# Kernel optimization log

Measured on AMD Instinct MI355X. Metric: run time of the kernel, lower is better.

Reference implementation:

```python
import jax, jax.numpy as jnp
import numpy as np

B, P, H = 256, 100, 512
NH, HD = 16, 32          # n_head, head_dim
V, N = 20, 200
VN = 1 + V + N           # 221
CSD = 16                 # cur_status_dim
SCALE = HD ** (-0.5)


def setup_inputs() -> dict:
    key = jax.random.key(0)
    ks = jax.random.split(key, 16)
    inp = {
        "q_global": jax.random.normal(ks[0], (B, P, H), jnp.float32),
        "k_global": jax.random.normal(ks[1], (B, NH, VN, HD), jnp.float32),
        "v_global": jax.random.normal(ks[2], (B, NH, VN, HD), jnp.float32),
        "k_node": jax.random.normal(ks[3], (B, NH, 1 + N, HD), jnp.float32),
        "v_node": jax.random.normal(ks[4], (B, NH, 1 + N, HD), jnp.float32),
        "k_vehicle": jax.random.normal(ks[5], (B, NH, 1 + V, HD), jnp.float32),
        "v_vehicle": jax.random.normal(ks[6], (B, NH, 1 + V, HD), jnp.float32),
        "k_vehicle_node": jax.random.normal(ks[7], (B, NH, V, HD), jnp.float32),
        "v_vehicle_node": jax.random.normal(ks[8], (B, NH, V, HD), jnp.float32),
        "context_feature": jax.random.normal(ks[9], (B, P, CSD), jnp.float32),
        "cache_pointer": jax.random.normal(ks[10], (B, H, VN), jnp.float32),
    }
    # random illegal mask; keep the depot column (0) always legal so no row is fully masked
    mask = jax.random.bernoulli(ks[11], 0.3, (B * P, VN))
    inp["illegal_mask"] = mask.at[:, 0].set(False)
    # learned params (torch Linear stores [out, in])
    inp["Wq_w"] = jax.random.normal(ks[12], (H, H + CSD), jnp.float32) * 0.02
    inp["combine_w"] = jax.random.normal(ks[13], (H, H), jnp.float32) * 0.02
    inp["combine_b"] = jax.random.normal(ks[14], (H,), jnp.float32) * 0.02
    return inp


def _attend(q, k, v, mask=None):
    # q: [B,NH,P,HD], k/v: [B,NH,K,HD], mask: [B,P,K] bool (True = illegal)
    scores = jnp.einsum("bhpd,bhkd->bhpk", q, k) * SCALE
    if mask is not None:
        scores = jnp.where(mask[:, None, :, :], -jnp.inf, scores)
    w = jax.nn.softmax(scores, axis=-1)
    ctx = jnp.einsum("bhpk,bhkd->bhpd", w, v)
    return ctx.transpose(0, 2, 1, 3).reshape(q.shape[0], q.shape[2], NH * HD)  # [B,P,H]


def reference(q_global, k_global, v_global, k_node, v_node, k_vehicle, v_vehicle,
              k_vehicle_node, v_vehicle_node, context_feature, cache_pointer,
              illegal_mask, Wq_w, combine_w, combine_b):
    mask = illegal_mask.reshape(B, P, VN)
    q = jnp.concatenate([q_global, context_feature], axis=-1) @ Wq_w.T  # [B,P,H]
    q = q.reshape(B, P, NH, HD).transpose(0, 2, 1, 3)                   # [B,NH,P,HD]
    context = (_attend(q, k_global, v_global, mask)
               + _attend(q, k_node, v_node)
               + _attend(q, k_vehicle, v_vehicle)
               + _attend(q, k_vehicle_node, v_vehicle_node))            # [B,P,H]
    mha_out = context @ combine_w.T + combine_b                          # [B,P,H]
    logits = jnp.einsum("bph,bhk->bpk", mha_out, cache_pointer)          # [B,P,VN]
    return logits.reshape(B * P, VN).astype(jnp.float32)
```

## Files before the change

kernel.cpp:

```cpp
#include <hip/hip_runtime.h>
#include <hip/hip_bf16.h>

#define B_   256
#define P_   100
#define H_   512
#define NH_  16
#define HD_  32
#define VN_  221
#define KNODE 201
#define KVEH  21
#define KVND  20
#define CSD_ 16
#define MASKP 224

typedef __attribute__((ext_vector_type(8))) short short8;
typedef __attribute__((ext_vector_type(4))) float f32x4;

#define K_OFF   0
#define V_OFF   38400
#define ATTN_LDS_B 69632

__device__ __forceinline__ unsigned cvtpk(float lo, float hi) {
    unsigned r;
    asm("v_cvt_pk_bf16_f32 %0, %1, %2" : "=v"(r) : "v"(lo), "v"(hi));
    return r;
}
__device__ __forceinline__ unsigned f2bf(float f) {
    union { float f; unsigned u; } x; x.f = f;
    return (x.u + 0x7FFFu + ((x.u >> 16) & 1u)) >> 16;
}

__global__ void mask_detect_kernel(const unsigned int* __restrict__ w,
                                   int nwords, int* __restrict__ flag) {
    int i = blockIdx.x * 256 + threadIdx.x;
    if (i < nwords && (w[i] & ~1u)) atomicOr(flag, 1);
}

__global__ void mask_repack_kernel(const unsigned char* __restrict__ mb,
                                   const int* __restrict__ mw,
                                   const int* __restrict__ flag,
                                   unsigned char* __restrict__ out) {
    int i = blockIdx.x * blockDim.x + threadIdx.x;
    if (i >= B_ * P_ * MASKP) return;
    int row = i / MASKP, k = i - row * MASKP;
    unsigned char v = 1;
    if (k < VN_) {
        int src = row * VN_ + k;
        v = (*flag) ? (unsigned char)(mb[src] != 0) : (unsigned char)(mw[src] != 0);
    }
    out[i] = v;
}

template<bool MASKED, int C0, int C1, int LO, int HI>
__device__ __forceinline__ void attend_v5(
    const char* __restrict__ ldsb,
    const unsigned* __restrict__ mpre,
    short8 qf, int g, int qr, int addrA, int addrB,
    f32x4& O0, f32x4& O1)
{
    f32x4 A0a = {0.f,0.f,0.f,0.f}, A1a = {0.f,0.f,0.f,0.f};
    f32x4 A0b = {0.f,0.f,0.f,0.f}, A1b = {0.f,0.f,0.f,0.f};
    float ssum = 0.f;
    const bool sel = g < 2;
    #pragma unroll
    for (int c = C0; c <= C1; ++c) {
        const int kb = c * 32;
        short8 kf0 = *(const short8*)(ldsb + K_OFF + (size_t)(kb + qr) * 80 + g * 16);
        short8 kf1 = *(const short8*)(ldsb + K_OFF + (size_t)(kb + 16 + qr) * 80 + g * 16);
        __builtin_amdgcn_s_setprio(1);
        f32x4 s0 = __builtin_amdgcn_mfma_f32_16x16x32_bf16(
                       kf0, qf, (f32x4){0.f,0.f,0.f,0.f}, 0, 0, 0);
        f32x4 s1 = __builtin_amdgcn_mfma_f32_16x16x32_bf16(
                       kf1, qf, (f32x4){0.f,0.f,0.f,0.f}, 0, 0, 0);
        __builtin_amdgcn_s_setprio(0);
        unsigned mdw0 = 0, mdw1 = 0;
        if (MASKED) {
            mdw0 = mpre[2 * (c - C0)];
            mdw1 = mpre[2 * (c - C0) + 1];
        }
        float e0[4], e1[4];
        #pragma unroll
        for (int r = 0; r < 4; ++r) {
            const int key0 = kb + 4 * g + r;
            const int key1 = key0 + 16;
            float x0 = exp2f(s0[r]);
            float x1 = exp2f(s1[r]);
            bool ok0, ok1;
            if (MASKED) {
                ok0 = ((mdw0 >> (8 * r)) & 255u) == 0u;
                ok1 = ((mdw1 >> (8 * r)) & 255u) == 0u;
            } else {
                ok0 = (key0 >= LO) & (key0 < HI);
                ok1 = (key1 >= LO) & (key1 < HI);
            }
            e0[r] = ok0 ? x0 : 0.f;
            e1[r] = ok1 ? x1 : 0.f;
            ssum += e0[r] + e1[r];
        }
        unsigned w0 = cvtpk(e0[0], e0[1]), w1 = cvtpk(e0[2], e0[3]);
        unsigned w2 = cvtpk(e1[0], e1[1]), w3 = cvtpk(e1[2], e1[3]);
        int pA0 = __builtin_amdgcn_ds_bpermute(addrA, (int)w0);
        int pA1 = __builtin_amdgcn_ds_bpermute(addrA, (int)w1);
        int pB0 = __builtin_amdgcn_ds_bpermute(addrB, (int)w0);
        int pB1 = __builtin_amdgcn_ds_bpermute(addrB, (int)w1);
        int qA0 = __builtin_amdgcn_ds_bpermute(addrA, (int)w2);
        int qA1 = __builtin_amdgcn_ds_bpermute(addrA, (int)w3);
        int qB0 = __builtin_amdgcn_ds_bpermute(addrB, (int)w2);
        int qB1 = __builtin_amdgcn_ds_bpermute(addrB, (int)w3);
        union { int u[4]; short8 s8; } pf;
        pf.u[0] = sel ? pA0 : qA0;
        pf.u[1] = sel ? pA1 : qA1;
        pf.u[2] = sel ? pB0 : qB0;
        pf.u[3] = sel ? pB1 : qB1;
        short8 v0 = *(const short8*)(ldsb + V_OFF + (size_t)qr * 976 + kb * 2 + g * 16);
        short8 v1 = *(const short8*)(ldsb + V_OFF + (size_t)(qr + 16) * 976 + kb * 2 + g * 16);
        __builtin_amdgcn_s_setprio(1);
        if (c & 1) {
            A0b = __builtin_amdgcn_mfma_f32_16x16x32_bf16(v0, pf.s8, A0b, 0, 0, 0);
            A1b = __builtin_amdgcn_mfma_f32_16x16x32_bf16(v1, pf.s8, A1b, 0, 0, 0);
        } else {
            A0a = __builtin_amdgcn_mfma_f32_16x16x32_bf16(v0, pf.s8, A0a, 0, 0, 0);
            A1a = __builtin_amdgcn_mfma_f32_16x16x32_bf16(v1, pf.s8, A1a, 0, 0, 0);
        }
        __builtin_amdgcn_s_setprio(0);
    }
    ssum += __shfl_xor(ssum, 16);
    ssum += __shfl_xor(ssum, 32);
    const float inv = 1.f / ssum;
    O0 += (A0a + A0b) * inv;
    O1 += (A1a + A1b) * inv;
}

__global__ __launch_bounds__(512, 4) void attn_mfma_kernel(
    const float* __restrict__ q4,
    const float* __restrict__ kg,  const float* __restrict__ vg,
    const float* __restrict__ kn,  const float* __restrict__ vn,
    const float* __restrict__ kv,  const float* __restrict__ vv,
    const float* __restrict__ kvn, const float* __restrict__ vvn,
    const unsigned char* __restrict__ maskp,
    float* __restrict__ ctx_out)
{
    extern __shared__ char ldsb[];
    const int tid = threadIdx.x;
    const int bh = blockIdx.x, b = bh >> 4, nh = bh & 15;

    const int wave = tid >> 6;
    const int g = (tid >> 4) & 3, qr = tid & 15;
    const int q0 = wave * 16;
    const int qe = (q0 + qr < 100) ? (q0 + qr) : 99;
    const float* qp = q4 + ((size_t)bh * 100 + qe) * 32 + g * 8;
    float4 qa = *(const float4*)qp;
    float4 qc = *(const float4*)(qp + 4);
    const unsigned char* mrow = maskp + ((size_t)b * 100 + qe) * MASKP;
    unsigned mpre[14];
    #pragma unroll
    for (int c = 0; c < 7; ++c) {
        mpre[2 * c]     = *(const unsigned*)(mrow + c * 32 + g * 4);
        mpre[2 * c + 1] = *(const unsigned*)(mrow + c * 32 + 16 + g * 4);
    }

    const float* kg_s  = kg  + (size_t)bh * VN_   * 32;
    const float* kn_s  = kn  + (size_t)bh * KNODE * 32;
    const float* kv_s  = kv  + (size_t)bh * KVEH  * 32;
    const float* kvn_s = kvn + (size_t)bh * KVND  * 32;
    const float* vg_s  = vg  + (size_t)bh * VN_   * 32;
    const float* vn_s  = vn  + (size_t)bh * KNODE * 32;
    const float* vv_s  = vv  + (size_t)bh * KVEH  * 32;
    const float* vvn_s = vvn + (size_t)bh * KVND  * 32;

    {
        float4 ka[4], kc[4];
        int koff[4]; bool kok[4];
        #pragma unroll
        for (int it = 0; it < 4; ++it) {
            int slot = tid + it * 512;
            kok[it] = slot < 1852;
            const float* sp; int li, r0;
            if (slot >= 1772)      { sp = kvn_s; li = slot - 1772; r0 = 456; }
            else if (slot >= 1688) { sp = kv_s;  li = slot - 1688; r0 = 432; }
            else if (slot >= 884)  { sp = kn_s;  li = slot - 884;  r0 = 224; }
            else                   { sp = kg_s;  li = slot;        r0 = 0;   }
            int r = li >> 2, s2 = li & 3;
            koff[it] = (r0 + r) * 80 + s2 * 16;
            if (kok[it]) {
                ka[it] = *(const float4*)(sp + r * 32 + s2 * 8);
                kc[it] = *(const float4*)(sp + r * 32 + s2 * 8 + 4);
            }
        }
        #pragma unroll
        for (int it = 0; it < 4; ++it) {
            if (kok[it]) {
                uint4 w;
                w.x = cvtpk(ka[it].x, ka[it].y); w.y = cvtpk(ka[it].z, ka[it].w);
                w.z = cvtpk(kc[it].x, kc[it].y); w.w = cvtpk(kc[it].z, kc[it].w);
                *(uint4*)(ldsb + K_OFF + koff[it]) = w;
            }
        }
    }
    for (int lin = tid; lin < 17 * 4; lin += 512) {
        int zi = lin >> 2, s = lin & 3;
        int zr = (zi < 3) ? 221 + zi : (zi < 10) ? 422 + zi
               : (zi < 13) ? 443 + zi : 463 + zi;
        *(uint4*)(ldsb + K_OFF + (size_t)zr * 80 + s * 16) = (uint4){0,0,0,0};
    }
    {
        char* vb = ldsb + V_OFF;
        float4 va[4], vb4[4];
        int vd0[4], vk2[4]; bool vok[4];
        #pragma unroll
        for (int it = 0; it < 4; ++it) {
            int slot = tid + it * 512;
            vok[it] = slot < 1840;
            const float* sp; int li, r0;
            if (slot >= 1760)      { sp = vvn_s; li = slot - 1760; r0 = 456; }
            else if (slot >= 1680) { sp = vv_s;  li = slot - 1680; r0 = 432; }
            else if (slot >= 880)  { sp = vn_s;  li = slot - 880;  r0 = 224; }
            else                   { sp = vg_s;  li = slot;        r0 = 0;   }
            int p = li >> 3, dq = li & 7;
            vd0[it] = dq * 4;
            vk2[it] = (r0 + 2 * p) * 2;
            if (vok[it]) {
                va[it]  = *(const float4*)(sp + (2 * p) * 32 + dq * 4);
                vb4[it] = *(const float4*)(sp + (2 * p + 1) * 32 + dq * 4);
            }
        }
        #pragma unroll
        for (int it = 0; it < 4; ++it) {
            if (vok[it]) {
                int d0 = vd0[it], k2 = vk2[it];
                *(unsigned*)(vb + (size_t)(d0 + 0) * 976 + k2) = cvtpk(va[it].x, vb4[it].x);
                *(unsigned*)(vb + (size_t)(d0 + 1) * 976 + k2) = cvtpk(va[it].y, vb4[it].y);
                *(unsigned*)(vb + (size_t)(d0 + 2) * 976 + k2) = cvtpk(va[it].z, vb4[it].z);
                *(unsigned*)(vb + (size_t)(d0 + 3) * 976 + k2) = cvtpk(va[it].w, vb4[it].w);
            }
        }
        if (tid < 32) {
            int d = tid;
            *(unsigned*)(vb + (size_t)d * 976 + 220 * 2) = cvtpk(vg_s[220 * 32 + d], 0.f);
            *(unsigned*)(vb + (size_t)d * 976 + 424 * 2) = cvtpk(vn_s[200 * 32 + d], 0.f);
            *(unsigned*)(vb + (size_t)d * 976 + 452 * 2) = cvtpk(vv_s[20 * 32 + d], 0.f);
        }
        for (int lin = tid; lin < 7 * 32; lin += 512) {
            int pi = lin >> 5, d = lin & 31;
            int pk = (pi == 0) ? 222 : (pi < 4) ? 424 + 2 * pi
                   : (pi == 4) ? 454 : 466 + 2 * pi;
            *(unsigned*)(vb + (size_t)d * 976 + (size_t)pk * 2) = 0;
        }
    }
    __syncthreads();

    if (wave >= 7) return;

    short8 qf;
    {
        const float SC = 0.2550524218f;
        union { unsigned u[4]; short8 s8; } q;
        q.u[0] = cvtpk(qa.x * SC, qa.y * SC);
        q.u[1] = cvtpk(qa.z * SC, qa.w * SC);
        q.u[2] = cvtpk(qc.x * SC, qc.y * SC);
        q.u[3] = cvtpk(qc.z * SC, qc.w * SC);
        qf = q.s8;
    }
    const int addrA = 4 * (qr + ((g & 1) << 5));
    const int addrB = addrA + 64;

    f32x4 O0 = {0.f,0.f,0.f,0.f}, O1 = {0.f,0.f,0.f,0.f};
    attend_v5<true,  0,  6,   0, 224>(ldsb, mpre, qf, g, qr, addrA, addrB, O0, O1);
    attend_v5<false, 7, 13, 224, 425>(ldsb, nullptr, qf, g, qr, addrA, addrB, O0, O1);
    attend_v5<false,13, 14, 432, 453>(ldsb, nullptr, qf, g, qr, addrA, addrB, O0, O1);
    attend_v5<false,14, 14, 456, 476>(ldsb, nullptr, qf, g, qr, addrA, addrB, O0, O1);

    if (q0 + qr < 100) {
        float* op = ctx_out + ((size_t)b * 100 + q0 + qr) * 512 + nh * 32 + 4 * g;
        *(f32x4*)op        = O0;
        *(f32x4*)(op + 16) = O1;
    }
}

template<bool QPROJ>
__global__ __launch_bounds__(512, 4) void gemm_nfused(
    const float* __restrict__ Aq, const float* __restrict__ cf,
    const float* __restrict__ W,  const float* __restrict__ bias,
    float* __restrict__ outp)
{
    __shared__ char As[64 * 80];
    __shared__ char Bs[256 * 80];
    const int tid = threadIdx.x;
    const int n0 = blockIdx.x * 256, m0 = blockIdx.y * 64;
    const int wave = tid >> 6, lane = tid & 63;
    const int wm = wave >> 2, wn = wave & 3;
    const int g = lane >> 4, qr = lane & 15;
    const int ar = tid >> 3, as = tid & 7;
    constexpr int KTOT_ = QPROJ ? 544 : 512;
    constexpr int WSTR  = QPROJ ? 528 : 512;

    f32x4 acc[2][4] = {};
    for (int k0 = 0; k0 < KTOT_; k0 += 32) {
        float4 a4 = {0,0,0,0};
        {
            const int k = k0 + as * 4;
            if (!QPROJ || k < 512) {
                a4 = *(const float4*)(Aq + (size_t)(m0 + ar) * 512 + k);
            } else if (k < 528) {
                a4 = *(const float4*)(cf + (size_t)(m0 + ar) * 16 + (k - 512));
            }
        }
        float4 b0[2], b1[2];
        #pragma unroll
        for (int it = 0; it < 2; ++it) {
            int slot = tid + it * 512;
            int row = slot >> 2, sq = slot & 3;
            int k = k0 + sq * 8;
            b0[it] = (float4){0,0,0,0}; b1[it] = (float4){0,0,0,0};
            if (!QPROJ || k < 528) {
                const float* wp = W + (size_t)(n0 + row) * WSTR + k;
                b0[it] = *(const float4*)wp;
                b1[it] = *(const float4*)(wp + 4);
            }
        }
        __syncthreads();
        {
            uint2 w;
            w.x = cvtpk(a4.x, a4.y); w.y = cvtpk(a4.z, a4.w);
            *(uint2*)(As + ar * 80 + as * 8) = w;
        }
        #pragma unroll
        for (int it = 0; it < 2; ++it) {
            int slot = tid + it * 512;
            int row = slot >> 2, sq = slot & 3;
            uint4 w;
            w.x = cvtpk(b0[it].x, b0[it].y); w.y = cvtpk(b0[it].z, b0[it].w);
            w.z = cvtpk(b1[it].x, b1[it].y); w.w = cvtpk(b1[it].z, b1[it].w);
            *(uint4*)(Bs + row * 80 + sq * 16) = w;
        }
        __syncthreads();
        short8 af0 = *(const short8*)(As + (wm * 32 + qr) * 80 + g * 16);
        short8 af1 = *(const short8*)(As + (wm * 32 + 16 + qr) * 80 + g * 16);
        #pragma unroll
        for (int nj = 0; nj < 4; ++nj) {
            short8 bf = *(const short8*)(Bs + (wn * 64 + nj * 16 + qr) * 80 + g * 16);
            acc[0][nj] = __builtin_amdgcn_mfma_f32_16x16x32_bf16(af0, bf, acc[0][nj], 0, 0, 0);
            acc[1][nj] = __builtin_amdgcn_mfma_f32_16x16x32_bf16(af1, bf, acc[1][nj], 0, 0, 0);
        }
    }
    #pragma unroll
    for (int mi = 0; mi < 2; ++mi)
        #pragma unroll
        for (int nj = 0; nj < 4; ++nj) {
            const int n = n0 + wn * 64 + nj * 16 + qr;
            const float bia = QPROJ ? 0.f : bias[n];
            #pragma unroll
            for (int reg = 0; reg < 4; ++reg) {
                int m = m0 + wm * 32 + 16 * mi + 4 * g + reg;
                if (QPROJ) {
                    int bb = m / 100, p = m - bb * 100;
                    int nh = n >> 5, d = n & 31;
                    outp[(((size_t)bb * NH_ + nh) * P_ + p) * HD_ + d] = acc[mi][nj][reg];
                } else {
                    outp[(size_t)m * 512 + n] = acc[mi][nj][reg] + bia;
                }
            }
        }
}

__global__ __launch_bounds__(512, 4) void logits_mfma(
    const float* __restrict__ mha,
    const float* __restrict__ cp,
    float* __restrict__ out)
{
    __shared__ char As[128 * 80];
    __shared__ char Bs[112 * 80];
    const int b   = blockIdx.x >> 1;
    const int nh0 = (blockIdx.x & 1) * 112;
    const int tid = threadIdx.x;
    const int wave = tid >> 6, lane = tid & 63;
    const int g = lane >> 4, qr = lane & 15;
    const int row = tid >> 2, s = tid & 3;

    f32x4 acc[7] = {};
    for (int h0 = 0; h0 < 512; h0 += 32) {
        float4 a4 = {0,0,0,0}, c4 = {0,0,0,0};
        if (row < 100) {
            const float* mp = mha + ((size_t)b * P_ + row) * 512 + h0 + 8 * s;
            a4 = *(const float4*)mp;
            c4 = *(const float4*)(mp + 4);
        }
        float cv[2][4];
        int ckk[2], chq[2]; bool cok[2];
        #pragma unroll
        for (int it = 0; it < 2; ++it) {
            int slot = tid + it * 512;
            bool in = slot < 896;
            int kkl = in ? (slot % 112) : 0;
            int hq  = in ? (slot / 112) : 0;
            int kk  = nh0 + kkl;
            ckk[it] = kkl; chq[it] = hq;
            cok[it] = in;
            cv[it][0] = cv[it][1] = cv[it][2] = cv[it][3] = 0.f;
            if (in && kk < VN_) {
                const float* cpp = cp + ((size_t)b * 512 + h0 + hq * 4) * VN_ + kk;
                cv[it][0] = cpp[0];
                cv[it][1] = cpp[VN_];
                cv[it][2] = cpp[2 * VN_];
                cv[it][3] = cpp[3 * VN_];
            }
        }
        __syncthreads();
        {
            uint4 w;
            w.x = cvtpk(a4.x, a4.y); w.y = cvtpk(a4.z, a4.w);
            w.z = cvtpk(c4.x, c4.y); w.w = cvtpk(c4.z, c4.w);
            *(uint4*)(As + row * 80 + s * 16) = w;
        }
        #pragma unroll
        for (int it = 0; it < 2; ++it) {
            if (cok[it]) {
                uint2 w;
                w.x = cvtpk(cv[it][0], cv[it][1]);
                w.y = cvtpk(cv[it][2], cv[it][3]);
                *(uint2*)(Bs + ckk[it] * 80 + chq[it] * 8) = w;
            }
        }
        __syncthreads();
        short8 af = *(const short8*)(As + (wave * 16 + qr) * 80 + g * 16);
        #pragma unroll
        for (int ni = 0; ni < 7; ++ni) {
            short8 bf = *(const short8*)(Bs + (ni * 16 + qr) * 80 + g * 16);
            acc[ni] = __builtin_amdgcn_mfma_f32_16x16x32_bf16(af, bf, acc[ni], 0, 0, 0);
        }
    }
    #pragma unroll
    for (int ni = 0; ni < 7; ++ni) {
        int key = nh0 + ni * 16 + qr;
        if (key >= VN_) continue;
        #pragma unroll
        for (int reg = 0; reg < 4; ++reg) {
            int p = wave * 16 + 4 * g + reg;
            if (p < P_)
                out[((size_t)b * P_ + p) * VN_ + key] = acc[ni][reg];
        }
    }
}

extern "C" void kernel_launch(void* const* d_in, const int* in_sizes, int n_in,
                              void* d_out, int out_size, void* d_ws, size_t ws_size,
                              hipStream_t stream) {
    const float* qg   = (const float*)d_in[0];
    const float* kgl  = (const float*)d_in[1];
    const float* vgl  = (const float*)d_in[2];
    const float* knd  = (const float*)d_in[3];
    const float* vnd  = (const float*)d_in[4];
    const float* kvh  = (const float*)d_in[5];
    const float* vvh  = (const float*)d_in[6];
    const float* kvnd = (const float*)d_in[7];
    const float* vvnd = (const float*)d_in[8];
    const float* cf   = (const float*)d_in[9];
    const float* cp   = (const float*)d_in[10];
    const void*  mask_raw = d_in[11];
    const float* Wq   = (const float*)d_in[12];
    const float* Wc   = (const float*)d_in[13];
    const float* bias = (const float*)d_in[14];
    float* out = (float*)d_out;

    const size_t NQ = (size_t)B_ * NH_ * P_ * HD_;
    float* q4buf  = (float*)d_ws;
    float* ctxbuf = q4buf + NQ;
    float* mhabuf = q4buf;
    unsigned char* mask8 = (unsigned char*)(ctxbuf + NQ);
    const int MASKN_P = B_ * P_ * MASKP;
    int* flag = (int*)(mask8 + ((MASKN_P + 15) & ~15));

    hipFuncSetAttribute(reinterpret_cast<const void*>(attn_mfma_kernel),
                        hipFuncAttributeMaxDynamicSharedMemorySize,
                        ATTN_LDS_B);

    hipMemsetAsync(flag, 0, sizeof(int), stream);
    mask_detect_kernel<<<16, 256, 0, stream>>>(
        (const unsigned int*)mask_raw, 4096, flag);
    mask_repack_kernel<<<(MASKN_P + 255) / 256, 256, 0, stream>>>(
        (const unsigned char*)mask_raw, (const int*)mask_raw, flag, mask8);

    gemm_nfused<true><<<dim3(2, 400), 512, 0, stream>>>(qg, cf, Wq, nullptr, q4buf);
    attn_mfma_kernel<<<B_ * NH_, 512, ATTN_LDS_B, stream>>>(
        q4buf, kgl, vgl, knd, vnd, kvh, vvh, kvnd, vvnd, mask8, ctxbuf);
    gemm_nfused<false><<<dim3(2, 400), 512, 0, stream>>>(ctxbuf, nullptr, Wc, bias, mhabuf);
    logits_mfma<<<B_ * 2, 512, 0, stream>>>(mhabuf, cp, out);
}
```

Measured before the change: 337.6 us.

## Make attention kernel persistent with warp-specialized double-buffered K/V prefetch

Replaces the one-block-per-(batch,head) attention launch with 256 persistent 1024-thread blocks that each loop over 16 (batch,head) tiles. Seven waves compute attention on the current LDS buffer while the other nine waves load and convert the next tile's K/V into a second LDS buffer, with one barrier per iteration. This aims to hide the global-load and bf16-conversion latency behind the MFMA work. The cost is double the LDS per block (about 136 KB), so only one block fits per CU. Only 256 blocks are launched, which may leave some CUs idle, and the loop adds a per-tile barrier.

```diff
diff --git a/kernel.cpp b/kernel.cpp
--- a/kernel.cpp
+++ b/kernel.cpp
@@ -19,6 +19,7 @@
 #define K_OFF   0
 #define V_OFF   38400
 #define ATTN_LDS_B 69632
+#define ATTN_LDS_2B (2 * ATTN_LDS_B)
 
 __device__ __forceinline__ unsigned cvtpk(float lo, float hi) {
     unsigned r;
@@ -131,7 +132,7 @@
     O1 += (A1a + A1b) * inv;
 }
 
-__global__ __launch_bounds__(512, 4) void attn_mfma_kernel(
+__global__ __launch_bounds__(1024, 4) void attn_ws(
     const float* __restrict__ q4,
     const float* __restrict__ kg,  const float* __restrict__ vg,
     const float* __restrict__ kn,  const float* __restrict__ vn,
@@ -140,40 +141,42 @@
     const unsigned char* __restrict__ maskp,
     float* __restrict__ ctx_out)
 {
-    extern __shared__ char ldsb[];
+    extern __shared__ char lds2[];
     const int tid = threadIdx.x;
-    const int bh = blockIdx.x, b = bh >> 4, nh = bh & 15;
-
-    const int wave = tid >> 6;
-    const int g = (tid >> 4) & 3, qr = tid & 15;
+    const int wave = tid >> 6, g = (tid >> 4) & 3, qr = tid & 15;
     const int q0 = wave * 16;
     const int qe = (q0 + qr < 100) ? (q0 + qr) : 99;
-    const float* qp = q4 + ((size_t)bh * 100 + qe) * 32 + g * 8;
-    float4 qa = *(const float4*)qp;
-    float4 qc = *(const float4*)(qp + 4);
-    const unsigned char* mrow = maskp + ((size_t)b * 100 + qe) * MASKP;
-    unsigned mpre[14];
+    const int addrA = 4 * (qr + ((g & 1) << 5));
+    const int addrB = addrA + 64;
+    const int t0i = blockIdx.x;
+
     #pragma unroll
-    for (int c = 0; c < 7; ++c) {
-        mpre[2 * c]     = *(const unsigned*)(mrow + c * 32 + g * 4);
-        mpre[2 * c + 1] = *(const unsigned*)(mrow + c * 32 + 16 + g * 4);
-    }
-
-    const float* kg_s  = kg  + (size_t)bh * VN_   * 32;
-    const float* kn_s  = kn  + (size_t)bh * KNODE * 32;
-    const float* kv_s  = kv  + (size_t)bh * KVEH  * 32;
-    const float* kvn_s = kvn + (size_t)bh * KVND  * 32;
-    const float* vg_s  = vg  + (size_t)bh * VN_   * 32;
-    const float* vn_s  = vn  + (size_t)bh * KNODE * 32;
-    const float* vv_s  = vv  + (size_t)bh * KVEH  * 32;
-    const float* vvn_s = vvn + (size_t)bh * KVND  * 32;
+    for (int bi = 0; bi < 2; ++bi) {
+        char* ldsb = lds2 + bi * ATTN_LDS_B;
+        if (tid < 68) {
+            int zi = tid >> 2, s = tid & 3;
+            int zr = (zi < 3) ? 221 + zi : (zi < 10) ? 422 + zi
+                   : (zi < 13) ? 443 + zi : 463 + zi;
+            *(uint4*)(ldsb + K_OFF + (size_t)zr * 80 + s * 16) = (uint4){0,0,0,0};
+        }
+        char* vb = ldsb + V_OFF;
+        if (tid < 224) {
+            int pi = tid >> 5, d = tid & 31;
+            int pk = (pi == 0) ? 222 : (pi < 4) ? 424 + 2 * pi
+                   : (pi == 4) ? 454 : 466 + 2 * pi;
+            *(unsigned*)(vb + (size_t)d * 976 + (size_t)pk * 2) = 0;
+        }
+    }
 
     {
-        float4 ka[4], kc[4];
-        int koff[4]; bool kok[4];
-        #pragma unroll
-        for (int it = 0; it < 4; ++it) {
-            int slot = tid + it * 512;
+        const float* kg_s  = kg  + (size_t)t0i * VN_   * 32;
+        const float* kn_s  = kn  + (size_t)t0i * KNODE * 32;
+        const float* kv_s  = kv  + (size_t)t0i * KVEH  * 32;
+        const float* kvn_s = kvn + (size_t)t0i * KVND  * 32;
+        float4 ka[2], kc[2]; int koff[2]; bool kok[2];
+        #pragma unroll
+        for (int it = 0; it < 2; ++it) {
+            int slot = tid + it * 1024;
             kok[it] = slot < 1852;
             const float* sp; int li, r0;
             if (slot >= 1772)      { sp = kvn_s; li = slot - 1772; r0 = 456; }
@@ -188,28 +191,23 @@
             }
         }
         #pragma unroll
-        for (int it = 0; it < 4; ++it) {
+        for (int it = 0; it < 2; ++it) {
             if (kok[it]) {
                 uint4 w;
                 w.x = cvtpk(ka[it].x, ka[it].y); w.y = cvtpk(ka[it].z, ka[it].w);
                 w.z = cvtpk(kc[it].x, kc[it].y); w.w = cvtpk(kc[it].z, kc[it].w);
-                *(uint4*)(ldsb + K_OFF + koff[it]) = w;
-            }
-        }
-    }
-    for (int lin = tid; lin < 17 * 4; lin += 512) {
-        int zi = lin >> 2, s = lin & 3;
-        int zr = (zi < 3) ? 221 + zi : (zi < 10) ? 422 + zi
-               : (zi < 13) ? 443 + zi : 463 + zi;
-        *(uint4*)(ldsb + K_OFF + (size_t)zr * 80 + s * 16) = (uint4){0,0,0,0};
-    }
-    {
-        char* vb = ldsb + V_OFF;
-        float4 va[4], vb4[4];
-        int vd0[4], vk2[4]; bool vok[4];
-        #pragma unroll
-        for (int it = 0; it < 4; ++it) {
-            int slot = tid + it * 512;
+                *(uint4*)(lds2 + K_OFF + koff[it]) = w;
+            }
+        }
+        const float* vg_s  = vg  + (size_t)t0i * VN_   * 32;
+        const float* vn_s  = vn  + (size_t)t0i * KNODE * 32;
+        const float* vv_s  = vv  + (size_t)t0i * KVEH  * 32;
+        const float* vvn_s = vvn + (size_t)t0i * KVND  * 32;
+        char* vb = lds2 + V_OFF;
+        float4 va[2], vc[2]; int vd0[2], vk2[2]; bool vok[2];
+        #pragma unroll
+        for (int it = 0; it < 2; ++it) {
+            int slot = tid + it * 1024;
             vok[it] = slot < 1840;
             const float* sp; int li, r0;
             if (slot >= 1760)      { sp = vvn_s; li = slot - 1760; r0 = 456; }
@@ -220,18 +218,18 @@
             vd0[it] = dq * 4;
             vk2[it] = (r0 + 2 * p) * 2;
             if (vok[it]) {
-                va[it]  = *(const float4*)(sp + (2 * p) * 32 + dq * 4);
-                vb4[it] = *(const float4*)(sp + (2 * p + 1) * 32 + dq * 4);
-            }
-        }
-        #pragma unroll
-        for (int it = 0; it < 4; ++it) {
+                va[it] = *(const float4*)(sp + (2 * p) * 32 + dq * 4);
+                vc[it] = *(const float4*)(sp + (2 * p + 1) * 32 + dq * 4);
+            }
+        }
+        #pragma unroll
+        for (int it = 0; it < 2; ++it) {
             if (vok[it]) {
                 int d0 = vd0[it], k2 = vk2[it];
-                *(unsigned*)(vb + (size_t)(d0 + 0) * 976 + k2) = cvtpk(va[it].x, vb4[it].x);
-                *(unsigned*)(vb + (size_t)(d0 + 1) * 976 + k2) = cvtpk(va[it].y, vb4[it].y);
-                *(unsigned*)(vb + (size_t)(d0 + 2) * 976 + k2) = cvtpk(va[it].z, vb4[it].z);
-                *(unsigned*)(vb + (size_t)(d0 + 3) * 976 + k2) = cvtpk(va[it].w, vb4[it].w);
+                *(unsigned*)(vb + (size_t)(d0 + 0) * 976 + k2) = cvtpk(va[it].x, vc[it].x);
+                *(unsigned*)(vb + (size_t)(d0 + 1) * 976 + k2) = cvtpk(va[it].y, vc[it].y);
+                *(unsigned*)(vb + (size_t)(d0 + 2) * 976 + k2) = cvtpk(va[it].z, vc[it].z);
+                *(unsigned*)(vb + (size_t)(d0 + 3) * 976 + k2) = cvtpk(va[it].w, vc[it].w);
             }
         }
         if (tid < 32) {
@@ -240,40 +238,127 @@
             *(unsigned*)(vb + (size_t)d * 976 + 424 * 2) = cvtpk(vn_s[200 * 32 + d], 0.f);
             *(unsigned*)(vb + (size_t)d * 976 + 452 * 2) = cvtpk(vv_s[20 * 32 + d], 0.f);
         }
-        for (int lin = tid; lin < 7 * 32; lin += 512) {
-            int pi = lin >> 5, d = lin & 31;
-            int pk = (pi == 0) ? 222 : (pi < 4) ? 424 + 2 * pi
-                   : (pi == 4) ? 454 : 466 + 2 * pi;
-            *(unsigned*)(vb + (size_t)d * 976 + (size_t)pk * 2) = 0;
-        }
     }
     __syncthreads();
 
-    if (wave >= 7) return;
-
-    short8 qf;
-    {
-        const float SC = 0.2550524218f;
-        union { unsigned u[4]; short8 s8; } q;
-        q.u[0] = cvtpk(qa.x * SC, qa.y * SC);
-        q.u[1] = cvtpk(qa.z * SC, qa.w * SC);
-        q.u[2] = cvtpk(qc.x * SC, qc.y * SC);
-        q.u[3] = cvtpk(qc.z * SC, qc.w * SC);
-        qf = q.s8;
-    }
-    const int addrA = 4 * (qr + ((g & 1) << 5));
-    const int addrB = addrA + 64;
-
-    f32x4 O0 = {0.f,0.f,0.f,0.f}, O1 = {0.f,0.f,0.f,0.f};
-    attend_v5<true,  0,  6,   0, 224>(ldsb, mpre, qf, g, qr, addrA, addrB, O0, O1);
-    attend_v5<false, 7, 13, 224, 425>(ldsb, nullptr, qf, g, qr, addrA, addrB, O0, O1);
-    attend_v5<false,13, 14, 432, 453>(ldsb, nullptr, qf, g, qr, addrA, addrB, O0, O1);
-    attend_v5<false,14, 14, 456, 476>(ldsb, nullptr, qf, g, qr, addrA, addrB, O0, O1);
-
-    if (q0 + qr < 100) {
-        float* op = ctx_out + ((size_t)b * 100 + q0 + qr) * 512 + nh * 32 + 4 * g;
-        *(f32x4*)op        = O0;
-        *(f32x4*)(op + 16) = O1;
+    int cur = 0;
+    #pragma unroll 1
+    for (int i = 0; i < 16; ++i) {
+        const int t = t0i + i * 256;
+        char* ldsc = lds2 + cur * ATTN_LDS_B;
+        char* ldsa = lds2 + (cur ^ 1) * ATTN_LDS_B;
+
+        if (wave < 7) {
+            const int b = t >> 4, nh = t & 15;
+            const float* qp = q4 + ((size_t)t * 100 + qe) * 32 + g * 8;
+            float4 qa = *(const float4*)qp;
+            float4 qc = *(const float4*)(qp + 4);
+            const unsigned char* mrow = maskp + ((size_t)b * 100 + qe) * MASKP;
+            unsigned mpre[14];
+            #pragma unroll
+            for (int c = 0; c < 7; ++c) {
+                mpre[2 * c]     = *(const unsigned*)(mrow + c * 32 + g * 4);
+                mpre[2 * c + 1] = *(const unsigned*)(mrow + c * 32 + 16 + g * 4);
+            }
+            short8 qf;
+            {
+                const float SC = 0.2550524218f;
+                union { unsigned u[4]; short8 s8; } q;
+                q.u[0] = cvtpk(qa.x * SC, qa.y * SC);
+                q.u[1] = cvtpk(qa.z * SC, qa.w * SC);
+                q.u[2] = cvtpk(qc.x * SC, qc.y * SC);
+                q.u[3] = cvtpk(qc.z * SC, qc.w * SC);
+                qf = q.s8;
+            }
+            f32x4 O0 = {0.f,0.f,0.f,0.f}, O1 = {0.f,0.f,0.f,0.f};
+            attend_v5<true,  0,  6,   0, 224>(ldsc, mpre, qf, g, qr, addrA, addrB, O0, O1);
+            attend_v5<false, 7, 13, 224, 425>(ldsc, nullptr, qf, g, qr, addrA, addrB, O0, O1);
+            attend_v5<false,13, 14, 432, 453>(ldsc, nullptr, qf, g, qr, addrA, addrB, O0, O1);
+            attend_v5<false,14, 14, 456, 476>(ldsc, nullptr, qf, g, qr, addrA, addrB, O0, O1);
+            if (q0 + qr < 100) {
+                float* op = ctx_out + ((size_t)b * 100 + q0 + qr) * 512 + nh * 32 + 4 * g;
+                *(f32x4*)op        = O0;
+                *(f32x4*)(op + 16) = O1;
+            }
+        } else if (i < 15) {
+            const int tn = t + 256;
+            const int ptid = tid - 448;
+            const float* kg_s  = kg  + (size_t)tn * VN_   * 32;
+            const float* kn_s  = kn  + (size_t)tn * KNODE * 32;
+            const float* kv_s  = kv  + (size_t)tn * KVEH  * 32;
+            const float* kvn_s = kvn + (size_t)tn * KVND  * 32;
+            {
+                float4 ka[4], kc[4]; int koff[4]; bool kok[4];
+                #pragma unroll
+                for (int it = 0; it < 4; ++it) {
+                    int slot = ptid + it * 576;
+                    kok[it] = slot < 1852;
+                    const float* sp; int li, r0;
+                    if (slot >= 1772)      { sp = kvn_s; li = slot - 1772; r0 = 456; }
+                    else if (slot >= 1688) { sp = kv_s;  li = slot - 1688; r0 = 432; }
+                    else if (slot >= 884)  { sp = kn_s;  li = slot - 884;  r0 = 224; }
+                    else                   { sp = kg_s;  li = slot;        r0 = 0;   }
+                    int r = li >> 2, s2 = li & 3;
+                    koff[it] = (r0 + r) * 80 + s2 * 16;
+                    if (kok[it]) {
+                        ka[it] = *(const float4*)(sp + r * 32 + s2 * 8);
+                        kc[it] = *(const float4*)(sp + r * 32 + s2 * 8 + 4);
+                    }
+                }
+                #pragma unroll
+                for (int it = 0; it < 4; ++it) {
+                    if (kok[it]) {
+                        uint4 w;
+                        w.x = cvtpk(ka[it].x, ka[it].y); w.y = cvtpk(ka[it].z, ka[it].w);
+                        w.z = cvtpk(kc[it].x, kc[it].y); w.w = cvtpk(kc[it].z, kc[it].w);
+                        *(uint4*)(ldsa + K_OFF + koff[it]) = w;
+                    }
+                }
+            }
+            {
+                const float* vg_s  = vg  + (size_t)tn * VN_   * 32;
+                const float* vn_s  = vn  + (size_t)tn * KNODE * 32;
+                const float* vv_s  = vv  + (size_t)tn * KVEH  * 32;
+                const float* vvn_s = vvn + (size_t)tn * KVND  * 32;
+                char* vb = ldsa + V_OFF;
+                float4 va[4], vc[4]; int vd0[4], vk2[4]; bool vok[4];
+                #pragma unroll
+                for (int it = 0; it < 4; ++it) {
+                    int slot = ptid + it * 576;
+                    vok[it] = slot < 1840;
+                    const float* sp; int li, r0;
+                    if (slot >= 1760)      { sp = vvn_s; li = slot - 1760; r0 = 456; }
+                    else if (slot >= 1680) { sp = vv_s;  li = slot - 1680; r0 = 432; }
+                    else if (slot >= 880)  { sp = vn_s;  li = slot - 880;  r0 = 224; }
+                    else                   { sp = vg_s;  li = slot;        r0 = 0;   }
+                    int p = li >> 3, dq = li & 7;
+                    vd0[it] = dq * 4;
+                    vk2[it] = (r0 + 2 * p) * 2;
+                    if (vok[it]) {
+                        va[it] = *(const float4*)(sp + (2 * p) * 32 + dq * 4);
+                        vc[it] = *(const float4*)(sp + (2 * p + 1) * 32 + dq * 4);
+                    }
+                }
+                #pragma unroll
+                for (int it = 0; it < 4; ++it) {
+                    if (vok[it]) {
+                        int d0 = vd0[it], k2 = vk2[it];
+                        *(unsigned*)(vb + (size_t)(d0 + 0) * 976 + k2) = cvtpk(va[it].x, vc[it].x);
+                        *(unsigned*)(vb + (size_t)(d0 + 1) * 976 + k2) = cvtpk(va[it].y, vc[it].y);
+                        *(unsigned*)(vb + (size_t)(d0 + 2) * 976 + k2) = cvtpk(va[it].z, vc[it].z);
+                        *(unsigned*)(vb + (size_t)(d0 + 3) * 976 + k2) = cvtpk(va[it].w, vc[it].w);
+                    }
+                }
+                if (ptid < 32) {
+                    int d = ptid;
+                    *(unsigned*)(vb + (size_t)d * 976 + 220 * 2) = cvtpk(vg_s[220 * 32 + d], 0.f);
+                    *(unsigned*)(vb + (size_t)d * 976 + 424 * 2) = cvtpk(vn_s[200 * 32 + d], 0.f);
+                    *(unsigned*)(vb + (size_t)d * 976 + 452 * 2) = cvtpk(vv_s[20 * 32 + d], 0.f);
+                }
+            }
+        }
+        __syncthreads();
+        cur ^= 1;
     }
 }
 
@@ -470,9 +555,9 @@
     const int MASKN_P = B_ * P_ * MASKP;
     int* flag = (int*)(mask8 + ((MASKN_P + 15) & ~15));
 
-    hipFuncSetAttribute(reinterpret_cast<const void*>(attn_mfma_kernel),
+    hipFuncSetAttribute(reinterpret_cast<const void*>(attn_ws),
                         hipFuncAttributeMaxDynamicSharedMemorySize,
-                        ATTN_LDS_B);
+                        ATTN_LDS_2B);
 
     hipMemsetAsync(flag, 0, sizeof(int), stream);
     mask_detect_kernel<<<16, 256, 0, stream>>>(
@@ -481,7 +566,7 @@
         (const unsigned char*)mask_raw, (const int*)mask_raw, flag, mask8);
 
     gemm_nfused<true><<<dim3(2, 400), 512, 0, stream>>>(qg, cf, Wq, nullptr, q4buf);
-    attn_mfma_kernel<<<B_ * NH_, 512, ATTN_LDS_B, stream>>>(
+    attn_ws<<<256, 1024, ATTN_LDS_2B, stream>>>(
         q4buf, kgl, vgl, knd, vnd, kvh, vvh, kvnd, vvnd, mask8, ctxbuf);
     gemm_nfused<false><<<dim3(2, 400), 512, 0, stream>>>(ctxbuf, nullptr, Wc, bias, mhabuf);
     logits_mfma<<<B_ * 2, 512, 0, stream>>>(mhabuf, cp, out);
```

Result: slower. 448.7 us (+32.9%).
